# Kernel tuning notes

Measured on AMD Instinct MI355X. Metric: run time of the kernel, lower is better.

## Reference

```python
import jax, jax.numpy as jnp
import numpy as np

W, HN, C, NHEAD = 256, 128, 512, 8


def layer_norm(x, w, b, eps=1e-5):
    m = x.mean(-1, keepdims=True)
    v = ((x - m) ** 2).mean(-1, keepdims=True)
    return (x - m) / jnp.sqrt(v + eps) * w + b


def setup_inputs() -> dict:
    key = jax.random.key(0)
    ks = jax.random.split(key, 6)
    s = 0.02
    return {
        "feat_left": jax.random.normal(ks[0], (W, HN, C), jnp.float32),
        "feat_right": jax.random.normal(ks[1], (W, HN, C), jnp.float32),
        "pos": jax.random.normal(ks[2], (2 * W - 1, C), jnp.float32),
        "pos_indexes": jax.random.randint(ks[3], (W * W,), 0, 2 * W - 1, dtype=jnp.int32),
        "ln_w": jnp.ones((C,), jnp.float32),
        "ln_b": jnp.zeros((C,), jnp.float32),
        "in_proj_w": jax.random.normal(ks[4], (3 * C, C), jnp.float32) * s,
        "in_proj_b": jnp.zeros((3 * C,), jnp.float32),
        "out_w": jax.random.normal(ks[5], (C, C), jnp.float32) * s,
        "out_b": jnp.zeros((C,), jnp.float32),
    }


def reference(feat_left, feat_right, pos, pos_indexes, ln_w, ln_b, in_proj_w, in_proj_b, out_w, out_b):
    w, n, c = feat_left.shape
    e = NHEAD
    hd = c // e
    scaling = hd ** -0.5

    # pre-norm (same norm1 applied to both streams)
    ql = layer_norm(feat_left, ln_w, ln_b)     # [W,N,C]
    kv_in = layer_norm(feat_right, ln_w, ln_b)  # [W,N,C]

    # cross-attn projections: q from left with in_proj[:C], k/v from right with in_proj[C:]
    q = ql @ in_proj_w[:c].T + in_proj_b[:c]
    kv = kv_in @ in_proj_w[c:].T + in_proj_b[c:]
    k, v = jnp.split(kv, 2, axis=-1)

    # relative pos encoding gather: [2W-1,C] -> [W*W,C] -> [W,W',C]
    pe = pos[pos_indexes].reshape(w, w, c)
    qr_kr = pe @ in_proj_w[: 2 * c].T + in_proj_b[: 2 * c]
    q_r, k_r = jnp.split(qr_kr, 2, axis=-1)

    q = (q * scaling).reshape(w, n, e, hd)
    q_r = (q_r * scaling).reshape(w, w, e, hd)
    k = k.reshape(w, n, e, hd)
    v = v.reshape(w, n, e, hd)
    k_r = k_r.reshape(w, w, e, hd)

    # content-content + content-pos + pos-content scores: [N,E,W,W']
    attn = (jnp.einsum('wnec,vnec->newv', q, k)
            + jnp.einsum('wnec,wvec->newv', q, k_r)
            + jnp.einsum('vnec,wvec->newv', k, q_r))

    raw_attn = attn.sum(axis=1)                      # [N,W,W']
    p = jax.nn.softmax(attn, axis=-1)
    v_o = jnp.einsum('newv,vnec->wnec', p, v).reshape(w, n, c)
    v_o = v_o @ out_w.T + out_b

    return feat_left + v_o, raw_attn
```

## Files before the change

kernel.cpp:

```cpp
#include <hip/hip_runtime.h>

#define WW 256
#define NB 128
#define CD 512
#define NE 8
#define HD 64
#define NCHUNKS 4
#define SCALING 0.125f

typedef __attribute__((ext_vector_type(8))) short bfx8;
typedef __attribute__((ext_vector_type(4))) float fx4;

#define OFF_MEAN   0u
#define OFF_RSTD   65536u
#define OFF_WPB    131072u
#define OFF_OWB    524288u
#define OFF_S      655360u
#define OFF_U      656896u
#define OFF_PQ     658432u
#define OFF_PK     789504u
#define OFF_QB     920576u
#define OFF_KB     9309184u
#define OFF_VB     17697792u
#define OFF_ATTN   26086400u
#define OFF_T3     42863616u
#define OFF_PB     51252224u

__device__ __forceinline__ unsigned short f2bf(float f) {
  unsigned u = __builtin_bit_cast(unsigned, f);
  u = (u + 0x7fffu + ((u >> 16) & 1u)) >> 16;
  return (unsigned short)u;
}
__device__ __forceinline__ float bf2f(unsigned short h) {
  unsigned u = ((unsigned)h) << 16;
  return __builtin_bit_cast(float, u);
}

#define GLDS16(g, l)                                                          \
  __builtin_amdgcn_global_load_lds(                                           \
      (const __attribute__((address_space(1))) void*)(g),                     \
      (__attribute__((address_space(3))) void*)(l), 16, 0, 0)

__global__ __launch_bounds__(256) void cvt_kernel(const float* __restrict__ a,
                                                  unsigned short* __restrict__ b,
                                                  int n8) {
  int i = blockIdx.x * 256 + threadIdx.x;
  if (i >= n8) return;
  float4 x = ((const float4*)a)[2 * i];
  float4 y = ((const float4*)a)[2 * i + 1];
  int4 o;
  o.x = (int)(((unsigned)f2bf(x.y) << 16) | f2bf(x.x));
  o.y = (int)(((unsigned)f2bf(x.w) << 16) | f2bf(x.z));
  o.z = (int)(((unsigned)f2bf(y.y) << 16) | f2bf(y.x));
  o.w = (int)(((unsigned)f2bf(y.w) << 16) | f2bf(y.z));
  ((int4*)b)[i] = o;
}

__global__ __launch_bounds__(256) void stats_kernel(const float* __restrict__ L,
                                                    const float* __restrict__ R,
                                                    float* __restrict__ mean,
                                                    float* __restrict__ rstd,
                                                    unsigned short* __restrict__ flb,
                                                    unsigned short* __restrict__ frb) {
  int wave = threadIdx.x >> 6, lane = threadIdx.x & 63;
  int base = (blockIdx.x * 4 + wave) * 4;
  float4 a[4], b[4];
#pragma unroll
  for (int r = 0; r < 4; ++r) {
    int row = base + r;
    const float* src = (row < 32768) ? (L + (size_t)row * CD) : (R + (size_t)(row - 32768) * CD);
    a[r] = *(const float4*)(src + lane * 4);
    b[r] = *(const float4*)(src + 256 + lane * 4);
  }
#pragma unroll
  for (int r = 0; r < 4; ++r) {
    int row = base + r;
    unsigned short* drow = (row < 32768) ? (flb + (size_t)row * CD) : (frb + (size_t)(row - 32768) * CD);
    short4 sa, sb;
    sa.x = (short)f2bf(a[r].x); sa.y = (short)f2bf(a[r].y); sa.z = (short)f2bf(a[r].z); sa.w = (short)f2bf(a[r].w);
    sb.x = (short)f2bf(b[r].x); sb.y = (short)f2bf(b[r].y); sb.z = (short)f2bf(b[r].z); sb.w = (short)f2bf(b[r].w);
    *(short4*)(drow + lane * 4) = sa;
    *(short4*)(drow + 256 + lane * 4) = sb;
  }
  float s[4], ss[4];
#pragma unroll
  for (int r = 0; r < 4; ++r) {
    s[r]  = a[r].x + a[r].y + a[r].z + a[r].w + b[r].x + b[r].y + b[r].z + b[r].w;
    ss[r] = a[r].x*a[r].x + a[r].y*a[r].y + a[r].z*a[r].z + a[r].w*a[r].w
          + b[r].x*b[r].x + b[r].y*b[r].y + b[r].z*b[r].z + b[r].w*b[r].w;
  }
#pragma unroll
  for (int off = 32; off > 0; off >>= 1)
#pragma unroll
    for (int r = 0; r < 4; ++r) {
      s[r]  += __shfl_xor(s[r], off);
      ss[r] += __shfl_xor(ss[r], off);
    }
  if (lane == 0) {
#pragma unroll
    for (int r = 0; r < 4; ++r) {
      float m = s[r] * (1.0f / 512.0f);
      float v = ss[r] * (1.0f / 512.0f) - m * m;
      mean[base + r] = m;
      rstd[base + r] = rsqrtf(v + 1e-5f);
    }
  }
}

__global__ __launch_bounds__(256) void prep_kernel(const float* __restrict__ ipw,
                                                   const float* __restrict__ ipb,
                                                   const float* __restrict__ lnw,
                                                   const float* __restrict__ lnb,
                                                   unsigned short* __restrict__ Wpb,
                                                   float* __restrict__ S,
                                                   float* __restrict__ U) {
  int o = blockIdx.x, t = threadIdx.x;
  float s = 0.f, u = 0.f;
#pragma unroll
  for (int j0 = 0; j0 < 512; j0 += 256) {
    int j = j0 + t;
    float w0 = ipw[(size_t)o * 512 + j];
    float wl = w0 * lnw[j];
    unsigned short h = f2bf(wl);
    Wpb[(size_t)o * 512 + j] = h;
    s += bf2f(h);
    u += w0 * lnb[j];
  }
  __shared__ float rs[4], ru[4];
  int lane = t & 63, wv = t >> 6;
#pragma unroll
  for (int off = 32; off > 0; off >>= 1) { s += __shfl_xor(s, off); u += __shfl_xor(u, off); }
  if (lane == 0) { rs[wv] = s; ru[wv] = u; }
  __syncthreads();
  if (t == 0) {
    S[o] = rs[0] + rs[1] + rs[2] + rs[3];
    U[o] = ru[0] + ru[1] + ru[2] + ru[3] + ipb[o];
  }
}

__global__ __launch_bounds__(256) void gemm_ln(const unsigned short* __restrict__ A,
                                               const unsigned short* __restrict__ Bw,
                                               const float* __restrict__ S,
                                               const float* __restrict__ U,
                                               const float* __restrict__ mean,
                                               const float* __restrict__ rstd,
                                               unsigned short* __restrict__ out0,
                                               unsigned short* __restrict__ out1,
                                               int wOff, int statOff, float scale) {
  __shared__ unsigned short As[2][128 * 32];
  __shared__ unsigned short Bs[2][128 * 32];
  int t = threadIdx.x;
  int lane = t & 63, w = t >> 6;
  int quad = lane >> 4, l15 = lane & 15;
  int wm = w >> 1, wn = w & 1;
  int m0 = blockIdx.x * 128, n0 = blockIdx.y * 128;

  int cs = ((lane & 3) ^ ((lane >> 3) & 3)) * 8;
  unsigned lo0 = (unsigned)(w * 16) * 32;
  unsigned lo1 = (unsigned)(64 + w * 16) * 32;
  const unsigned short* gA0 = A + (size_t)(m0 + w * 16 + (lane >> 2)) * 512 + cs;
  const unsigned short* gA1 = gA0 + (size_t)64 * 512;
  const unsigned short* gB0 = Bw + (size_t)(wOff + n0 + w * 16 + (lane >> 2)) * 512 + cs;
  const unsigned short* gB1 = gB0 + (size_t)64 * 512;

  fx4 acc[4][4];
#pragma unroll
  for (int i = 0; i < 4; ++i)
#pragma unroll
    for (int j = 0; j < 4; ++j) acc[i][j] = (fx4){0.f, 0.f, 0.f, 0.f};

  int ro = (quad ^ ((l15 >> 1) & 3)) * 8;

#define STAGE_G(buf, kk)                                                      \
  do {                                                                        \
    GLDS16(gA0 + (kk), &As[buf][lo0]);                                        \
    GLDS16(gA1 + (kk), &As[buf][lo1]);                                        \
    GLDS16(gB0 + (kk), &Bs[buf][lo0]);                                        \
    GLDS16(gB1 + (kk), &Bs[buf][lo1]);                                        \
  } while (0)

#define COMPUTE_G(buf)                                                        \
  do {                                                                        \
    const unsigned short* Ab = &As[buf][0];                                   \
    const unsigned short* Bb = &Bs[buf][0];                                   \
    bfx8 af[4], bfr[4];                                                       \
    _Pragma("unroll")                                                         \
    for (int i = 0; i < 4; ++i)                                               \
      af[i] = *(const bfx8*)(Ab + (size_t)(wm * 64 + i * 16 + l15) * 32 + ro);\
    _Pragma("unroll")                                                         \
    for (int j = 0; j < 4; ++j)                                               \
      bfr[j] = *(const bfx8*)(Bb + (size_t)(wn * 64 + j * 16 + l15) * 32 + ro);\
    _Pragma("unroll")                                                         \
    for (int i = 0; i < 4; ++i)                                               \
      _Pragma("unroll")                                                       \
      for (int j = 0; j < 4; ++j)                                             \
        acc[i][j] = __builtin_amdgcn_mfma_f32_16x16x32_bf16(af[i], bfr[j], acc[i][j], 0, 0, 0); \
  } while (0)

  STAGE_G(0, 0);
  int cur = 0;
  for (int kt = 0; kt < 480; kt += 32) {
    STAGE_G(cur ^ 1, kt + 32);
    asm volatile("s_waitcnt vmcnt(4)" ::: "memory");
    __builtin_amdgcn_s_barrier();
    __builtin_amdgcn_sched_barrier(0);
    COMPUTE_G(cur);
    asm volatile("s_waitcnt lgkmcnt(0)" ::: "memory");
    __builtin_amdgcn_s_barrier();
    __builtin_amdgcn_sched_barrier(0);
    cur ^= 1;
  }
  asm volatile("s_waitcnt vmcnt(0)" ::: "memory");
  __builtin_amdgcn_s_barrier();
  __builtin_amdgcn_sched_barrier(0);
  COMPUTE_G(cur);

  float mn[16], rs[16];
#pragma unroll
  for (int i = 0; i < 4; ++i)
#pragma unroll
    for (int r = 0; r < 4; ++r) {
      int m = statOff + m0 + wm * 64 + i * 16 + quad * 4 + r;
      mn[i * 4 + r] = mean[m];
      rs[i * 4 + r] = rstd[m];
    }
#pragma unroll
  for (int j = 0; j < 4; ++j) {
    int oc = n0 + wn * 64 + j * 16 + l15;
    int o = wOff + oc;
    float Sv = S[o], Uv = U[o];
    unsigned short* dst; int cc;
    if (oc < 512) { dst = out0; cc = oc; } else { dst = out1; cc = oc - 512; }
#pragma unroll
    for (int i = 0; i < 4; ++i)
#pragma unroll
      for (int r = 0; r < 4; ++r) {
        int m = m0 + wm * 64 + i * 16 + quad * 4 + r;
        dst[(size_t)m * 512 + cc] =
            f2bf(((acc[i][j][r] - mn[i * 4 + r] * Sv) * rs[i * 4 + r] + Uv) * scale);
      }
  }
#undef STAGE_G
#undef COMPUTE_G
}

__global__ __launch_bounds__(256) void gemm_out(const unsigned short* __restrict__ A,
                                                const unsigned short* __restrict__ Bw,
                                                const float* __restrict__ ob,
                                                const float* __restrict__ fl,
                                                float* __restrict__ out) {
  __shared__ unsigned short As[2][128 * 32];
  __shared__ unsigned short Bs[2][128 * 32];
  int t = threadIdx.x;
  int lane = t & 63, w = t >> 6;
  int quad = lane >> 4, l15 = lane & 15;
  int wm = w >> 1, wn = w & 1;
  int n0 = blockIdx.x * 128, m0 = blockIdx.y * 128;

  int cs = ((lane & 3) ^ ((lane >> 3) & 3)) * 8;
  unsigned lo0 = (unsigned)(w * 16) * 32;
  unsigned lo1 = (unsigned)(64 + w * 16) * 32;
  const unsigned short* gA0 = A + (size_t)(m0 + w * 16 + (lane >> 2)) * 512 + cs;
  const unsigned short* gA1 = gA0 + (size_t)64 * 512;
  const unsigned short* gB0 = Bw + (size_t)(n0 + w * 16 + (lane >> 2)) * 512 + cs;
  const unsigned short* gB1 = gB0 + (size_t)64 * 512;

  fx4 acc[4][4];
#pragma unroll
  for (int i = 0; i < 4; ++i)
#pragma unroll
    for (int j = 0; j < 4; ++j) acc[i][j] = (fx4){0.f, 0.f, 0.f, 0.f};

  int ro = (quad ^ ((l15 >> 1) & 3)) * 8;

#define STAGE_O(buf, kk)                                                      \
  do {                                                                        \
    GLDS16(gA0 + (kk), &As[buf][lo0]);                                        \
    GLDS16(gA1 + (kk), &As[buf][lo1]);                                        \
    GLDS16(gB0 + (kk), &Bs[buf][lo0]);                                        \
    GLDS16(gB1 + (kk), &Bs[buf][lo1]);                                        \
  } while (0)

#define COMPUTE_O(buf)                                                        \
  do {                                                                        \
    const unsigned short* Ab = &As[buf][0];                                   \
    const unsigned short* Bb = &Bs[buf][0];                                   \
    bfx8 af[4], bfr[4];                                                       \
    _Pragma("unroll")                                                         \
    for (int i = 0; i < 4; ++i)                                               \
      af[i] = *(const bfx8*)(Ab + (size_t)(wm * 64 + i * 16 + l15) * 32 + ro);\
    _Pragma("unroll")                                                         \
    for (int j = 0; j < 4; ++j)                                               \
      bfr[j] = *(const bfx8*)(Bb + (size_t)(wn * 64 + j * 16 + l15) * 32 + ro);\
    _Pragma("unroll")                                                         \
    for (int i = 0; i < 4; ++i)                                               \
      _Pragma("unroll")                                                       \
      for (int j = 0; j < 4; ++j)                                             \
        acc[i][j] = __builtin_amdgcn_mfma_f32_16x16x32_bf16(af[i], bfr[j], acc[i][j], 0, 0, 0); \
  } while (0)

  STAGE_O(0, 0);
  int cur = 0;
  for (int kt = 0; kt < 480; kt += 32) {
    STAGE_O(cur ^ 1, kt + 32);
    asm volatile("s_waitcnt vmcnt(4)" ::: "memory");
    __builtin_amdgcn_s_barrier();
    __builtin_amdgcn_sched_barrier(0);
    COMPUTE_O(cur);
    asm volatile("s_waitcnt lgkmcnt(0)" ::: "memory");
    __builtin_amdgcn_s_barrier();
    __builtin_amdgcn_sched_barrier(0);
    cur ^= 1;
  }
  asm volatile("s_waitcnt vmcnt(0)" ::: "memory");
  __builtin_amdgcn_s_barrier();
  __builtin_amdgcn_sched_barrier(0);
  COMPUTE_O(cur);

#pragma unroll
  for (int j = 0; j < 4; ++j) {
    int o = n0 + wn * 64 + j * 16 + l15;
    float bias = ob[o];
#pragma unroll
    for (int i = 0; i < 4; ++i)
#pragma unroll
      for (int r = 0; r < 4; ++r) {
        int m = m0 + wm * 64 + i * 16 + quad * 4 + r;
        size_t go = (size_t)m * 512 + o;
        out[go] = acc[i][j][r] + bias + fl[go];
      }
  }
#undef STAGE_O
#undef COMPUTE_O
}

__global__ __launch_bounds__(256) void posproj_mfma(const unsigned short* __restrict__ Apos,
                                                    const unsigned short* __restrict__ Bw,
                                                    const float* __restrict__ ipb,
                                                    unsigned short* __restrict__ Pq,
                                                    unsigned short* __restrict__ Pk) {
  __shared__ unsigned short As[2][128 * 32];
  __shared__ unsigned short Bs[2][128 * 32];
  int t = threadIdx.x;
  int lane = t & 63, w = t >> 6;
  int quad = lane >> 4, l15 = lane & 15;
  int wm = w >> 1, wn = w & 1;
  int m0 = blockIdx.x * 128, n0 = blockIdx.y * 128;

  int cs = ((lane & 3) ^ ((lane >> 3) & 3)) * 8;
  unsigned lo0 = (unsigned)(w * 16) * 32;
  unsigned lo1 = (unsigned)(64 + w * 16) * 32;
  int ar0 = m0 + w * 16 + (lane >> 2); if (ar0 > 510) ar0 = 510;
  int ar1 = m0 + 64 + w * 16 + (lane >> 2); if (ar1 > 510) ar1 = 510;
  const unsigned short* gA0 = Apos + (size_t)ar0 * 512 + cs;
  const unsigned short* gA1 = Apos + (size_t)ar1 * 512 + cs;
  const unsigned short* gB0 = Bw + (size_t)(n0 + w * 16 + (lane >> 2)) * 512 + cs;
  const unsigned short* gB1 = gB0 + (size_t)64 * 512;

  fx4 acc[4][4];
#pragma unroll
  for (int i = 0; i < 4; ++i)
#pragma unroll
    for (int j = 0; j < 4; ++j) acc[i][j] = (fx4){0.f, 0.f, 0.f, 0.f};

  int ro = (quad ^ ((l15 >> 1) & 3)) * 8;

#define STAGE_P(buf, kk)                                                      \
  do {                                                                        \
    GLDS16(gA0 + (kk), &As[buf][lo0]);                                        \
    GLDS16(gA1 + (kk), &As[buf][lo1]);                                        \
    GLDS16(gB0 + (kk), &Bs[buf][lo0]);                                        \
    GLDS16(gB1 + (kk), &Bs[buf][lo1]);                                        \
  } while (0)

#define COMPUTE_P(buf)                                                        \
  do {                                                                        \
    const unsigned short* Ab = &As[buf][0];                                   \
    const unsigned short* Bb = &Bs[buf][0];                                   \
    bfx8 af[4], bfr[4];                                                       \
    _Pragma("unroll")                                                         \
    for (int i = 0; i < 4; ++i)                                               \
      af[i] = *(const bfx8*)(Ab + (size_t)(wm * 64 + i * 16 + l15) * 32 + ro);\
    _Pragma("unroll")                                                         \
    for (int j = 0; j < 4; ++j)                                               \
      bfr[j] = *(const bfx8*)(Bb + (size_t)(wn * 64 + j * 16 + l15) * 32 + ro);\
    _Pragma("unroll")                                                         \
    for (int i = 0; i < 4; ++i)                                               \
      _Pragma("unroll")                                                       \
      for (int j = 0; j < 4; ++j)                                             \
        acc[i][j] = __builtin_amdgcn_mfma_f32_16x16x32_bf16(af[i], bfr[j], acc[i][j], 0, 0, 0); \
  } while (0)

  STAGE_P(0, 0);
  int cur = 0;
  for (int kt = 0; kt < 480; kt += 32) {
    STAGE_P(cur ^ 1, kt + 32);
    asm volatile("s_waitcnt vmcnt(4)" ::: "memory");
    __builtin_amdgcn_s_barrier();
    __builtin_amdgcn_sched_barrier(0);
    COMPUTE_P(cur);
    asm volatile("s_waitcnt lgkmcnt(0)" ::: "memory");
    __builtin_amdgcn_s_barrier();
    __builtin_amdgcn_sched_barrier(0);
    cur ^= 1;
  }
  asm volatile("s_waitcnt vmcnt(0)" ::: "memory");
  __builtin_amdgcn_s_barrier();
  __builtin_amdgcn_sched_barrier(0);
  COMPUTE_P(cur);

#pragma unroll
  for (int j = 0; j < 4; ++j) {
    int o = n0 + wn * 64 + j * 16 + l15;
    float bias = ipb[o];
    float scale = (o < 512) ? SCALING : 1.0f;
    unsigned short* dst; int cc;
    if (o < 512) { dst = Pq; cc = o; } else { dst = Pk; cc = o - 512; }
#pragma unroll
    for (int i = 0; i < 4; ++i)
#pragma unroll
      for (int r = 0; r < 4; ++r) {
        int m = m0 + wm * 64 + i * 16 + quad * 4 + r;
        if (m < 511)
          dst[(size_t)m * 512 + cc] = f2bf((acc[i][j][r] + bias) * scale);
      }
  }
#undef STAGE_P
#undef COMPUTE_P
}

__global__ __launch_bounds__(256) void t3_kernel(const unsigned short* __restrict__ kb,
                                                 const unsigned short* __restrict__ Pq,
                                                 const int* __restrict__ idx,
                                                 unsigned short* __restrict__ T3, int wc) {
  __shared__ unsigned short As[128 * 72];
  __shared__ unsigned short Bs[64 * 72];
  int t = threadIdx.x, lane = t & 63, w = t >> 6;
  int quad = lane >> 4, l15 = lane & 15;
  int e = blockIdx.x, v = blockIdx.y;
  const unsigned short* asrc = kb + ((size_t)v * NB) * 512 + e * 64;
  for (int c = t; c < 1024; c += 256) {
    int row = c >> 3, c8 = c & 7;
    *(int4*)(As + row * 72 + c8 * 8) = *(const int4*)(asrc + (size_t)row * 512 + c8 * 8);
  }
  for (int c = t; c < 512; c += 256) {
    int row = c >> 3, c8 = c & 7;
    int ri = idx[(wc * 64 + row) * WW + v];
    *(int4*)(Bs + row * 72 + c8 * 8) = *(const int4*)(Pq + (size_t)ri * 512 + e * 64 + c8 * 8);
  }
  __syncthreads();
  fx4 acc[2][4];
#pragma unroll
  for (int i = 0; i < 2; ++i)
#pragma unroll
    for (int j = 0; j < 4; ++j) acc[i][j] = (fx4){0.f, 0.f, 0.f, 0.f};
#pragma unroll
  for (int kt = 0; kt < 64; kt += 32) {
    bfx8 af[2], bfr[4];
#pragma unroll
    for (int i = 0; i < 2; ++i)
      af[i] = *(const bfx8*)(As + (w * 32 + i * 16 + l15) * 72 + kt + quad * 8);
#pragma unroll
    for (int j = 0; j < 4; ++j)
      bfr[j] = *(const bfx8*)(Bs + (j * 16 + l15) * 72 + kt + quad * 8);
#pragma unroll
    for (int i = 0; i < 2; ++i)
#pragma unroll
      for (int j = 0; j < 4; ++j)
        acc[i][j] = __builtin_amdgcn_mfma_f32_16x16x32_bf16(af[i], bfr[j], acc[i][j], 0, 0, 0);
  }
#pragma unroll
  for (int i = 0; i < 2; ++i)
#pragma unroll
    for (int j = 0; j < 4; ++j)
#pragma unroll
      for (int r = 0; r < 4; ++r) {
        int n = w * 32 + i * 16 + quad * 4 + r;
        int wq = j * 16 + l15;
        T3[(((size_t)e * WW + v) * NB + n) * 64 + wq] = f2bf(acc[i][j][r]);
      }
}

__global__ __launch_bounds__(256) void t1_kernel(const unsigned short* __restrict__ qb,
                                                 const unsigned short* __restrict__ kb,
                                                 const unsigned short* __restrict__ T3,
                                                 unsigned short* __restrict__ attnb, int wc) {
  __shared__ unsigned short As[64 * 72];
  __shared__ unsigned short Bs[256 * 72];
  int t = threadIdx.x, lane = t & 63, w = t >> 6;
  int quad = lane >> 4, l15 = lane & 15;
  int e = blockIdx.x, n = blockIdx.y;
  const unsigned short* asrc = qb + ((size_t)(wc * 64) * NB + n) * 512 + e * 64;
  for (int c = t; c < 512; c += 256) {
    int row = c >> 3, c8 = c & 7;
    *(int4*)(As + row * 72 + c8 * 8) = *(const int4*)(asrc + (size_t)row * NB * 512 + c8 * 8);
  }
  const unsigned short* bsrc = kb + (size_t)n * 512 + e * 64;
  for (int c = t; c < 2048; c += 256) {
    int row = c >> 3, c8 = c & 7;
    *(int4*)(Bs + row * 72 + c8 * 8) = *(const int4*)(bsrc + (size_t)row * NB * 512 + c8 * 8);
  }
  __syncthreads();
  fx4 acc[4][4];
#pragma unroll
  for (int i = 0; i < 4; ++i)
#pragma unroll
    for (int j = 0; j < 4; ++j) acc[i][j] = (fx4){0.f, 0.f, 0.f, 0.f};
#pragma unroll
  for (int kt = 0; kt < 64; kt += 32) {
    bfx8 af[4], bfr[4];
#pragma unroll
    for (int i = 0; i < 4; ++i)
      af[i] = *(const bfx8*)(As + (i * 16 + l15) * 72 + kt + quad * 8);
#pragma unroll
    for (int j = 0; j < 4; ++j)
      bfr[j] = *(const bfx8*)(Bs + (w * 64 + j * 16 + l15) * 72 + kt + quad * 8);
#pragma unroll
    for (int i = 0; i < 4; ++i)
#pragma unroll
      for (int j = 0; j < 4; ++j)
        acc[i][j] = __builtin_amdgcn_mfma_f32_16x16x32_bf16(af[i], bfr[j], acc[i][j], 0, 0, 0);
  }
  __syncthreads();
  const unsigned short* tsrc = T3 + ((size_t)e * WW * NB + n) * 64;
  for (int c = t; c < 2048; c += 256) {
    int row = c >> 3, c8 = c & 7;
    *(int4*)(Bs + row * 72 + c8 * 8) = *(const int4*)(tsrc + (size_t)row * NB * 64 + c8 * 8);
  }
  __syncthreads();
#pragma unroll
  for (int i = 0; i < 4; ++i)
#pragma unroll
    for (int j = 0; j < 4; ++j) {
      int vg = w * 64 + j * 16 + l15;
      ushort4 t3v = *(const ushort4*)(Bs + (size_t)vg * 72 + i * 16 + quad * 4);
      const unsigned short tv[4] = {t3v.x, t3v.y, t3v.z, t3v.w};
#pragma unroll
      for (int r = 0; r < 4; ++r) {
        int wq = i * 16 + quad * 4 + r;
        attnb[(((size_t)n * NE + e) * 64 + wq) * WW + vg] = f2bf(acc[i][j][r] + bf2f(tv[r]));
      }
    }
}

__global__ __launch_bounds__(256) void t2s_kernel(const unsigned short* __restrict__ qb,
                                                  const unsigned short* __restrict__ Pk,
                                                  const int* __restrict__ idx,
                                                  const unsigned short* __restrict__ attnb,
                                                  unsigned short* __restrict__ pbuf,
                                                  float* __restrict__ raw, int wc) {
  __shared__ unsigned short As[16 * 72];
  __shared__ unsigned short Bs[256 * 72];
  __shared__ int idxs[256];
  __shared__ float redm[16 * 4];
  __shared__ float reds[16 * 4];
  int t = threadIdx.x, lane = t & 63, w = t >> 6;
  int quad = lane >> 4, l15 = lane & 15;
  int wq = blockIdx.x, nt = blockIdx.y;
  int n0 = nt * 16;
  idxs[t] = idx[((size_t)(wc * 64 + wq)) * WW + t];

  fx4 raws[4];
#pragma unroll
  for (int j = 0; j < 4; ++j) raws[j] = (fx4){0.f, 0.f, 0.f, 0.f};

  const unsigned short* abase = qb + ((size_t)(wc * 64 + wq) * NB + n0) * 512;

  for (int e = 0; e < NE; ++e) {
    __syncthreads();
    if (t < 128) {
      int row = t >> 3, c8 = t & 7;
      *(int4*)(As + row * 72 + c8 * 8) = *(const int4*)(abase + (size_t)row * 512 + e * 64 + c8 * 8);
    }
    for (int c = t; c < 2048; c += 256) {
      int row = c >> 3, c8 = c & 7;
      int ri = idxs[row];
      *(int4*)(Bs + row * 72 + c8 * 8) = *(const int4*)(Pk + (size_t)ri * 512 + e * 64 + c8 * 8);
    }
    __syncthreads();

    fx4 acc[4];
#pragma unroll
    for (int j = 0; j < 4; ++j) acc[j] = (fx4){0.f, 0.f, 0.f, 0.f};
    bfx8 af0 = *(const bfx8*)(As + l15 * 72 + quad * 8);
    bfx8 af1 = *(const bfx8*)(As + l15 * 72 + 32 + quad * 8);
#pragma unroll
    for (int j = 0; j < 4; ++j) {
      bfx8 b0 = *(const bfx8*)(Bs + (w * 64 + j * 16 + l15) * 72 + quad * 8);
      acc[j] = __builtin_amdgcn_mfma_f32_16x16x32_bf16(af0, b0, acc[j], 0, 0, 0);
    }
#pragma unroll
    for (int j = 0; j < 4; ++j) {
      bfx8 b1 = *(const bfx8*)(Bs + (w * 64 + j * 16 + l15) * 72 + 32 + quad * 8);
      acc[j] = __builtin_amdgcn_mfma_f32_16x16x32_bf16(af1, b1, acc[j], 0, 0, 0);
    }

#pragma unroll
    for (int j = 0; j < 4; ++j) {
      int vg = w * 64 + j * 16 + l15;
#pragma unroll
      for (int r = 0; r < 4; ++r) {
        int n = n0 + quad * 4 + r;
        acc[j][r] += bf2f(attnb[(((size_t)n * NE + e) * 64 + wq) * WW + vg]);
      }
    }

    float rm[4];
#pragma unroll
    for (int r = 0; r < 4; ++r)
      rm[r] = fmaxf(fmaxf(acc[0][r], acc[1][r]), fmaxf(acc[2][r], acc[3][r]));
#pragma unroll
    for (int off = 1; off < 16; off <<= 1)
#pragma unroll
      for (int r = 0; r < 4; ++r) rm[r] = fmaxf(rm[r], __shfl_xor(rm[r], off));
    if (l15 == 0) {
#pragma unroll
      for (int r = 0; r < 4; ++r) redm[(quad * 4 + r) * 4 + w] = rm[r];
    }
    __syncthreads();
    float fm[4];
#pragma unroll
    for (int r = 0; r < 4; ++r) {
      const float* rp = redm + (quad * 4 + r) * 4;
      fm[r] = fmaxf(fmaxf(rp[0], rp[1]), fmaxf(rp[2], rp[3]));
    }
    float ex[4][4];
    float ls[4] = {0.f, 0.f, 0.f, 0.f};
#pragma unroll
    for (int j = 0; j < 4; ++j)
#pragma unroll
      for (int r = 0; r < 4; ++r) {
        ex[j][r] = __expf(acc[j][r] - fm[r]);
        ls[r] += ex[j][r];
      }
#pragma unroll
    for (int off = 1; off < 16; off <<= 1)
#pragma unroll
      for (int r = 0; r < 4; ++r) ls[r] += __shfl_xor(ls[r], off);
    if (l15 == 0) {
#pragma unroll
      for (int r = 0; r < 4; ++r) reds[(quad * 4 + r) * 4 + w] = ls[r];
    }
    __syncthreads();
    float inv[4];
#pragma unroll
    for (int r = 0; r < 4; ++r) {
      const float* sp = reds + (quad * 4 + r) * 4;
      inv[r] = 1.0f / (sp[0] + sp[1] + sp[2] + sp[3]);
    }
#pragma unroll
    for (int j = 0; j < 4; ++j) {
      int vg = w * 64 + j * 16 + l15;
#pragma unroll
      for (int r = 0; r < 4; ++r) {
        int n = n0 + quad * 4 + r;
        pbuf[(((size_t)n * NE + e) * 64 + wq) * WW + vg] = f2bf(ex[j][r] * inv[r]);
        raws[j][r] += acc[j][r];
      }
    }
  }

#pragma unroll
  for (int j = 0; j < 4; ++j) {
    int vg = w * 64 + j * 16 + l15;
#pragma unroll
    for (int r = 0; r < 4; ++r) {
      int n = n0 + quad * 4 + r;
      raw[((size_t)n * WW + wc * 64 + wq) * WW + vg] = raws[j][r];
    }
  }
}

__global__ __launch_bounds__(256) void pv_kernel(const unsigned short* __restrict__ pb,
                                                 const unsigned short* __restrict__ vb,
                                                 unsigned short* __restrict__ vob) {
  __shared__ unsigned short As[64 * 72];
  __shared__ unsigned short Bs[64 * 72];
  int t = threadIdx.x, lane = t & 63, w = t >> 6;
  int quad = lane >> 4, l15 = lane & 15;
  int e = blockIdx.x, n = blockIdx.y;
  fx4 acc[4];
#pragma unroll
  for (int j = 0; j < 4; ++j) acc[j] = (fx4){0.f, 0.f, 0.f, 0.f};
  const unsigned short* abase = pb + (((size_t)n * NE + e) * 64) * WW;
  for (int kc = 0; kc < 4; ++kc) {
    for (int c = t; c < 512; c += 256) {
      int row = c >> 3, c8 = c & 7;
      *(int4*)(As + row * 72 + c8 * 8) = *(const int4*)(abase + (size_t)row * WW + kc * 64 + c8 * 8);
    }
    for (int c = t; c < 512; c += 256) {
      int row = c >> 3, c8 = c & 7;
      *(int4*)(Bs + row * 72 + c8 * 8) =
          *(const int4*)(vb + ((size_t)(kc * 64 + row) * NB + n) * 512 + e * 64 + c8 * 8);
    }
    __syncthreads();
#pragma unroll
    for (int kt = 0; kt < 64; kt += 32) {
      bfx8 af = *(const bfx8*)(As + (w * 16 + l15) * 72 + kt + quad * 8);
      bfx8 bfr[4];
#pragma unroll
      for (int j = 0; j < 4; ++j)
        bfr[j] = *(const bfx8*)(Bs + (j * 16 + l15) * 72 + kt + quad * 8);
#pragma unroll
      for (int j = 0; j < 4; ++j)
        acc[j] = __builtin_amdgcn_mfma_f32_16x16x32_bf16(af, bfr[j], acc[j], 0, 0, 0);
    }
    __syncthreads();
  }
#pragma unroll
  for (int j = 0; j < 4; ++j)
#pragma unroll
    for (int r = 0; r < 4; ++r) {
      int wq = w * 16 + quad * 4 + r;
      vob[((size_t)wq * NB + n) * 512 + e * 64 + j * 16 + l15] = f2bf(acc[j][r]);
    }
}

extern "C" void kernel_launch(void* const* d_in, const int* in_sizes, int n_in,
                              void* d_out, int out_size, void* d_ws, size_t ws_size,
                              hipStream_t stream) {
  const float* fl  = (const float*)d_in[0];
  const float* fr  = (const float*)d_in[1];
  const float* pos = (const float*)d_in[2];
  const int*  pidx = (const int*)d_in[3];
  const float* lnw = (const float*)d_in[4];
  const float* lnb = (const float*)d_in[5];
  const float* ipw = (const float*)d_in[6];
  const float* ipb = (const float*)d_in[7];
  const float* ow  = (const float*)d_in[8];
  const float* ob  = (const float*)d_in[9];

  float* ws   = (float*)d_ws;
  float* mean = ws + OFF_MEAN;
  float* rstd = ws + OFF_RSTD;
  unsigned short* Wpb = (unsigned short*)(ws + OFF_WPB);
  unsigned short* owb = (unsigned short*)(ws + OFF_OWB);
  float* S    = ws + OFF_S;
  float* U    = ws + OFF_U;
  unsigned short* Pq = (unsigned short*)(ws + OFF_PQ);
  unsigned short* Pk = (unsigned short*)(ws + OFF_PK);
  unsigned short* qb = (unsigned short*)(ws + OFF_QB);
  unsigned short* kb = (unsigned short*)(ws + OFF_KB);
  unsigned short* vb = (unsigned short*)(ws + OFF_VB);
  unsigned short* attnb = (unsigned short*)(ws + OFF_ATTN);
  unsigned short* vob4  = attnb + (size_t)16777216;
  unsigned short* T3  = (unsigned short*)(ws + OFF_T3);
  unsigned short* pb  = (unsigned short*)(ws + OFF_PB);
  unsigned short* flb = (unsigned short*)(ws + OFF_ATTN);
  unsigned short* frb = flb + (size_t)32768 * 512;
  unsigned short* posb = (unsigned short*)(ws + OFF_T3);
  unsigned short* ipwb = posb + 262144;

  float* outF = (float*)d_out;
  float* outR = outF + (size_t)WW * NB * CD;

  stats_kernel<<<4096, 256, 0, stream>>>(fl, fr, mean, rstd, flb, frb);
  prep_kernel<<<1536, 256, 0, stream>>>(ipw, ipb, lnw, lnb, Wpb, S, U);
  cvt_kernel<<<128, 256, 0, stream>>>(ow, owb, 32768);
  cvt_kernel<<<128, 256, 0, stream>>>(pos, posb, 32704);
  cvt_kernel<<<256, 256, 0, stream>>>(ipw, ipwb, 65536);
  posproj_mfma<<<dim3(4, 8), 256, 0, stream>>>(posb, ipwb, ipb, Pq, Pk);
  gemm_ln<<<dim3(256, 4), 256, 0, stream>>>(flb, Wpb, S, U, mean, rstd, qb, qb, 0, 0, SCALING);
  gemm_ln<<<dim3(256, 8), 256, 0, stream>>>(frb, Wpb, S, U, mean, rstd, kb, vb, 512, 32768, 1.0f);

  for (int wc = 0; wc < NCHUNKS; ++wc) {
    t3_kernel<<<dim3(8, 256), 256, 0, stream>>>(kb, Pq, pidx, T3, wc);
    t1_kernel<<<dim3(8, 128), 256, 0, stream>>>(qb, kb, T3, attnb, wc);
    t2s_kernel<<<dim3(64, 8), 256, 0, stream>>>(qb, Pk, pidx, attnb, pb, outR, wc);
    pv_kernel<<<dim3(8, 128), 256, 0, stream>>>(pb, vb, vob4 + (size_t)wc * 64 * NB * 512);
  }
  gemm_out<<<dim3(4, 256), 256, 0, stream>>>(vob4, owb, ob, fl, outF);
}
```

Before: 770.4 us.

## Fuse layernorm stats and bf16 conversion into input-projection GEMM A-loads

Drops the separate stats kernel that read fp32 features, wrote bf16 copies and per-row mean/rstd. The projection GEMM now loads fp32 A tiles into registers, converts them to bf16 into swizzled LDS, and accumulates row sums and sums of squares on the way. Stats are reduced by shuffles into shared memory for the epilogue. This removes a kernel launch and a bf16 round-trip through global memory. The cost is that blocks sharing an M tile (4 or 8 N-blocks) each re-read fp32 A at twice the bytes and redo the conversion, and the pipeline now uses register staging in place of direct global-to-LDS loads.

```diff
diff --git a/kernel.cpp b/kernel.cpp
--- a/kernel.cpp
+++ b/kernel.cpp
@@ -11,8 +11,6 @@
 typedef __attribute__((ext_vector_type(8))) short bfx8;
 typedef __attribute__((ext_vector_type(4))) float fx4;
 
-#define OFF_MEAN   0u
-#define OFF_RSTD   65536u
 #define OFF_WPB    131072u
 #define OFF_OWB    524288u
 #define OFF_S      655360u
@@ -35,6 +33,9 @@
   unsigned u = ((unsigned)h) << 16;
   return __builtin_bit_cast(float, u);
 }
+__device__ __forceinline__ int packbf(float lo, float hi) {
+  return (int)(((unsigned)f2bf(hi) << 16) | f2bf(lo));
+}
 
 #define GLDS16(g, l)                                                          \
   __builtin_amdgcn_global_load_lds(                                           \
@@ -49,62 +50,11 @@
   float4 x = ((const float4*)a)[2 * i];
   float4 y = ((const float4*)a)[2 * i + 1];
   int4 o;
-  o.x = (int)(((unsigned)f2bf(x.y) << 16) | f2bf(x.x));
-  o.y = (int)(((unsigned)f2bf(x.w) << 16) | f2bf(x.z));
-  o.z = (int)(((unsigned)f2bf(y.y) << 16) | f2bf(y.x));
-  o.w = (int)(((unsigned)f2bf(y.w) << 16) | f2bf(y.z));
+  o.x = packbf(x.x, x.y);
+  o.y = packbf(x.z, x.w);
+  o.z = packbf(y.x, y.y);
+  o.w = packbf(y.z, y.w);
   ((int4*)b)[i] = o;
-}
-
-__global__ __launch_bounds__(256) void stats_kernel(const float* __restrict__ L,
-                                                    const float* __restrict__ R,
-                                                    float* __restrict__ mean,
-                                                    float* __restrict__ rstd,
-                                                    unsigned short* __restrict__ flb,
-                                                    unsigned short* __restrict__ frb) {
-  int wave = threadIdx.x >> 6, lane = threadIdx.x & 63;
-  int base = (blockIdx.x * 4 + wave) * 4;
-  float4 a[4], b[4];
-#pragma unroll
-  for (int r = 0; r < 4; ++r) {
-    int row = base + r;
-    const float* src = (row < 32768) ? (L + (size_t)row * CD) : (R + (size_t)(row - 32768) * CD);
-    a[r] = *(const float4*)(src + lane * 4);
-    b[r] = *(const float4*)(src + 256 + lane * 4);
-  }
-#pragma unroll
-  for (int r = 0; r < 4; ++r) {
-    int row = base + r;
-    unsigned short* drow = (row < 32768) ? (flb + (size_t)row * CD) : (frb + (size_t)(row - 32768) * CD);
-    short4 sa, sb;
-    sa.x = (short)f2bf(a[r].x); sa.y = (short)f2bf(a[r].y); sa.z = (short)f2bf(a[r].z); sa.w = (short)f2bf(a[r].w);
-    sb.x = (short)f2bf(b[r].x); sb.y = (short)f2bf(b[r].y); sb.z = (short)f2bf(b[r].z); sb.w = (short)f2bf(b[r].w);
-    *(short4*)(drow + lane * 4) = sa;
-    *(short4*)(drow + 256 + lane * 4) = sb;
-  }
-  float s[4], ss[4];
-#pragma unroll
-  for (int r = 0; r < 4; ++r) {
-    s[r]  = a[r].x + a[r].y + a[r].z + a[r].w + b[r].x + b[r].y + b[r].z + b[r].w;
-    ss[r] = a[r].x*a[r].x + a[r].y*a[r].y + a[r].z*a[r].z + a[r].w*a[r].w
-          + b[r].x*b[r].x + b[r].y*b[r].y + b[r].z*b[r].z + b[r].w*b[r].w;
-  }
-#pragma unroll
-  for (int off = 32; off > 0; off >>= 1)
-#pragma unroll
-    for (int r = 0; r < 4; ++r) {
-      s[r]  += __shfl_xor(s[r], off);
-      ss[r] += __shfl_xor(ss[r], off);
-    }
-  if (lane == 0) {
-#pragma unroll
-    for (int r = 0; r < 4; ++r) {
-      float m = s[r] * (1.0f / 512.0f);
-      float v = ss[r] * (1.0f / 512.0f) - m * m;
-      mean[base + r] = m;
-      rstd[base + r] = rsqrtf(v + 1e-5f);
-    }
-  }
 }
 
 __global__ __launch_bounds__(256) void prep_kernel(const float* __restrict__ ipw,
@@ -138,28 +88,32 @@
   }
 }
 
-__global__ __launch_bounds__(256) void gemm_ln(const unsigned short* __restrict__ A,
+__global__ __launch_bounds__(256) void gemm_ln(const float* __restrict__ A,
                                                const unsigned short* __restrict__ Bw,
                                                const float* __restrict__ S,
                                                const float* __restrict__ U,
-                                               const float* __restrict__ mean,
-                                               const float* __restrict__ rstd,
                                                unsigned short* __restrict__ out0,
                                                unsigned short* __restrict__ out1,
-                                               int wOff, int statOff, float scale) {
+                                               int wOff, float scale) {
   __shared__ unsigned short As[2][128 * 32];
   __shared__ unsigned short Bs[2][128 * 32];
+  __shared__ float sm[128], sv[128];
   int t = threadIdx.x;
   int lane = t & 63, w = t >> 6;
   int quad = lane >> 4, l15 = lane & 15;
   int wm = w >> 1, wn = w & 1;
   int m0 = blockIdx.x * 128, n0 = blockIdx.y * 128;
 
-  int cs = ((lane & 3) ^ ((lane >> 3) & 3)) * 8;
+  int swz = (lane & 3) ^ ((lane >> 3) & 3);
+  int row0 = w * 16 + (lane >> 2);
+  unsigned aw0 = (unsigned)row0 * 32 + swz * 8;
+  unsigned aw1 = aw0 + 64 * 32;
   unsigned lo0 = (unsigned)(w * 16) * 32;
   unsigned lo1 = (unsigned)(64 + w * 16) * 32;
-  const unsigned short* gA0 = A + (size_t)(m0 + w * 16 + (lane >> 2)) * 512 + cs;
-  const unsigned short* gA1 = gA0 + (size_t)64 * 512;
+
+  const float* gA0 = A + (size_t)(m0 + row0) * 512 + (lane & 3) * 8;
+  const float* gA1 = gA0 + (size_t)64 * 512;
+  int cs = swz * 8;
   const unsigned short* gB0 = Bw + (size_t)(wOff + n0 + w * 16 + (lane >> 2)) * 512 + cs;
   const unsigned short* gB1 = gB0 + (size_t)64 * 512;
 
@@ -171,10 +125,36 @@
 
   int ro = (quad ^ ((l15 >> 1) & 3)) * 8;
 
-#define STAGE_G(buf, kk)                                                      \
+  float4 a00, a01, a10, a11;
+  float s0 = 0.f, ss0 = 0.f, s1 = 0.f, ss1 = 0.f;
+
+#define LOADA(kk)                                                             \
   do {                                                                        \
-    GLDS16(gA0 + (kk), &As[buf][lo0]);                                        \
-    GLDS16(gA1 + (kk), &As[buf][lo1]);                                        \
+    a00 = *(const float4*)(gA0 + (kk));                                       \
+    a01 = *(const float4*)(gA0 + (kk) + 4);                                   \
+    a10 = *(const float4*)(gA1 + (kk));                                       \
+    a11 = *(const float4*)(gA1 + (kk) + 4);                                   \
+  } while (0)
+
+#define CVTSTATS(buf)                                                         \
+  do {                                                                        \
+    int4 w0v, w1v;                                                            \
+    w0v.x = packbf(a00.x, a00.y); w0v.y = packbf(a00.z, a00.w);               \
+    w0v.z = packbf(a01.x, a01.y); w0v.w = packbf(a01.z, a01.w);               \
+    w1v.x = packbf(a10.x, a10.y); w1v.y = packbf(a10.z, a10.w);               \
+    w1v.z = packbf(a11.x, a11.y); w1v.w = packbf(a11.z, a11.w);               \
+    *(int4*)(&As[buf][aw0]) = w0v;                                            \
+    *(int4*)(&As[buf][aw1]) = w1v;                                            \
+    s0 += a00.x + a00.y + a00.z + a00.w + a01.x + a01.y + a01.z + a01.w;      \
+    ss0 += a00.x*a00.x + a00.y*a00.y + a00.z*a00.z + a00.w*a00.w              \
+         + a01.x*a01.x + a01.y*a01.y + a01.z*a01.z + a01.w*a01.w;             \
+    s1 += a10.x + a10.y + a10.z + a10.w + a11.x + a11.y + a11.z + a11.w;      \
+    ss1 += a10.x*a10.x + a10.y*a10.y + a10.z*a10.z + a10.w*a10.w              \
+         + a11.x*a11.x + a11.y*a11.y + a11.z*a11.z + a11.w*a11.w;             \
+  } while (0)
+
+#define GLDSB(buf, kk)                                                        \
+  do {                                                                        \
     GLDS16(gB0 + (kk), &Bs[buf][lo0]);                                        \
     GLDS16(gB1 + (kk), &Bs[buf][lo1]);                                        \
   } while (0)
@@ -197,32 +177,57 @@
         acc[i][j] = __builtin_amdgcn_mfma_f32_16x16x32_bf16(af[i], bfr[j], acc[i][j], 0, 0, 0); \
   } while (0)
 
-  STAGE_G(0, 0);
+  LOADA(0);
+  __builtin_amdgcn_sched_barrier(0);
+  GLDSB(0, 0);
+  __builtin_amdgcn_sched_barrier(0);
   int cur = 0;
   for (int kt = 0; kt < 480; kt += 32) {
-    STAGE_G(cur ^ 1, kt + 32);
-    asm volatile("s_waitcnt vmcnt(4)" ::: "memory");
+    asm volatile("s_waitcnt vmcnt(2)" ::: "memory");
+    CVTSTATS(cur);
+    __builtin_amdgcn_sched_barrier(0);
+    LOADA(kt + 32);
+    __builtin_amdgcn_sched_barrier(0);
+    GLDSB(cur ^ 1, kt + 32);
+    __builtin_amdgcn_sched_barrier(0);
+    asm volatile("s_waitcnt vmcnt(6) lgkmcnt(0)" ::: "memory");
     __builtin_amdgcn_s_barrier();
     __builtin_amdgcn_sched_barrier(0);
     COMPUTE_G(cur);
-    asm volatile("s_waitcnt lgkmcnt(0)" ::: "memory");
     __builtin_amdgcn_s_barrier();
     __builtin_amdgcn_sched_barrier(0);
     cur ^= 1;
   }
-  asm volatile("s_waitcnt vmcnt(0)" ::: "memory");
+  asm volatile("s_waitcnt vmcnt(2)" ::: "memory");
+  CVTSTATS(cur);
+  __builtin_amdgcn_sched_barrier(0);
+  asm volatile("s_waitcnt vmcnt(0) lgkmcnt(0)" ::: "memory");
   __builtin_amdgcn_s_barrier();
   __builtin_amdgcn_sched_barrier(0);
   COMPUTE_G(cur);
 
+  s0 += __shfl_xor(s0, 1); s0 += __shfl_xor(s0, 2);
+  ss0 += __shfl_xor(ss0, 1); ss0 += __shfl_xor(ss0, 2);
+  s1 += __shfl_xor(s1, 1); s1 += __shfl_xor(s1, 2);
+  ss1 += __shfl_xor(ss1, 1); ss1 += __shfl_xor(ss1, 2);
+  if ((lane & 3) == 0) {
+    float m0v = s0 * (1.0f / 512.0f);
+    float v0v = ss0 * (1.0f / 512.0f) - m0v * m0v;
+    sm[row0] = m0v; sv[row0] = rsqrtf(v0v + 1e-5f);
+    float m1v = s1 * (1.0f / 512.0f);
+    float v1v = ss1 * (1.0f / 512.0f) - m1v * m1v;
+    sm[row0 + 64] = m1v; sv[row0 + 64] = rsqrtf(v1v + 1e-5f);
+  }
+  __syncthreads();
+
   float mn[16], rs[16];
 #pragma unroll
   for (int i = 0; i < 4; ++i)
 #pragma unroll
     for (int r = 0; r < 4; ++r) {
-      int m = statOff + m0 + wm * 64 + i * 16 + quad * 4 + r;
-      mn[i * 4 + r] = mean[m];
-      rs[i * 4 + r] = rstd[m];
+      int ml = wm * 64 + i * 16 + quad * 4 + r;
+      mn[i * 4 + r] = sm[ml];
+      rs[i * 4 + r] = sv[ml];
     }
 #pragma unroll
   for (int j = 0; j < 4; ++j) {
@@ -240,7 +245,9 @@
             f2bf(((acc[i][j][r] - mn[i * 4 + r] * Sv) * rs[i * 4 + r] + Uv) * scale);
       }
   }
-#undef STAGE_G
+#undef LOADA
+#undef CVTSTATS
+#undef GLDSB
 #undef COMPUTE_G
 }
 
@@ -731,8 +738,6 @@
   const float* ob  = (const float*)d_in[9];
 
   float* ws   = (float*)d_ws;
-  float* mean = ws + OFF_MEAN;
-  float* rstd = ws + OFF_RSTD;
   unsigned short* Wpb = (unsigned short*)(ws + OFF_WPB);
   unsigned short* owb = (unsigned short*)(ws + OFF_OWB);
   float* S    = ws + OFF_S;
@@ -746,22 +751,19 @@
   unsigned short* vob4  = attnb + (size_t)16777216;
   unsigned short* T3  = (unsigned short*)(ws + OFF_T3);
   unsigned short* pb  = (unsigned short*)(ws + OFF_PB);
-  unsigned short* flb = (unsigned short*)(ws + OFF_ATTN);
-  unsigned short* frb = flb + (size_t)32768 * 512;
   unsigned short* posb = (unsigned short*)(ws + OFF_T3);
   unsigned short* ipwb = posb + 262144;
 
   float* outF = (float*)d_out;
   float* outR = outF + (size_t)WW * NB * CD;
 
-  stats_kernel<<<4096, 256, 0, stream>>>(fl, fr, mean, rstd, flb, frb);
   prep_kernel<<<1536, 256, 0, stream>>>(ipw, ipb, lnw, lnb, Wpb, S, U);
   cvt_kernel<<<128, 256, 0, stream>>>(ow, owb, 32768);
   cvt_kernel<<<128, 256, 0, stream>>>(pos, posb, 32704);
   cvt_kernel<<<256, 256, 0, stream>>>(ipw, ipwb, 65536);
   posproj_mfma<<<dim3(4, 8), 256, 0, stream>>>(posb, ipwb, ipb, Pq, Pk);
-  gemm_ln<<<dim3(256, 4), 256, 0, stream>>>(flb, Wpb, S, U, mean, rstd, qb, qb, 0, 0, SCALING);
-  gemm_ln<<<dim3(256, 8), 256, 0, stream>>>(frb, Wpb, S, U, mean, rstd, kb, vb, 512, 32768, 1.0f);
+  gemm_ln<<<dim3(256, 4), 256, 0, stream>>>(fl, Wpb, S, U, qb, qb, 0, SCALING);
+  gemm_ln<<<dim3(256, 8), 256, 0, stream>>>(fr, Wpb, S, U, kb, vb, 512, 1.0f);
 
   for (int wc = 0; wc < NCHUNKS; ++wc) {
     t3_kernel<<<dim3(8, 256), 256, 0, stream>>>(kb, Pq, pidx, T3, wc);
```

Result: no change. 785.6 us (+2.0%).
